# Performance work log

Hardware: AMD Instinct MI355X
Metric: run time of the kernel (lower is better)

The kernel has to match this reference:

```python
import jax, jax.numpy as jnp
import numpy as np

# Model constants (from opt / init_kwargs)
DELTT = 5.0          # temporal resolution [s]
N_TIME = 60          # number of time frames
TR = 5.0             # repetition time
FA = 10.0            # flip angle [deg]
R1 = 4.5             # contrast-agent relaxivity
EPS = 1e-8
SCALE_KTRANS = 1.0
SCALE_VP = 1.0
SCALE_VE = 1.0


def setup_inputs() -> dict:
    key = jax.random.key(0)
    k1, k2, k3, k4 = jax.random.split(key, 4)
    B, T, H, W = 8, N_TIME, 256, 256
    return {
        "params": jax.random.uniform(k1, (B, 3, H, W), dtype=jnp.float32),
        "Cp": jax.random.uniform(k2, (B, T), dtype=jnp.float32),
        "S0": jax.random.uniform(k3, (B, 1, H, W), dtype=jnp.float32),
        "T1": jax.random.uniform(k4, (B, 1, H, W), dtype=jnp.float32),
    }


def reference(params, Cp, S0, T1):
    # PK parameter maps, each [B,1,H,W]
    Ktrans = params[:, 0:1] / SCALE_KTRANS / 60.0
    vp = params[:, 1:2] / SCALE_VP
    ve = params[:, 2:3] / SCALE_VE
    Kep = Ktrans / (ve + EPS)

    # The original O(T^2) windowed sum
    #   Ce[n] = sum_{m<=n} Cp[m] * exp(-Kep*(n-m)*dt) * dt
    # collapses to the linear recurrence
    #   Ce[n] = Ce[n-1]*exp(-Kep*dt) + Cp[n]*dt
    decay = jnp.exp(-Kep[:, 0] * DELTT)  # [B,H,W]

    def step(c, cp_t):
        c = c * decay + cp_t[:, None, None] * DELTT
        return c, c

    c0 = jnp.zeros_like(decay)
    _, Ce = jax.lax.scan(step, c0, Cp.T)   # [T,B,H,W]
    Ce = jnp.moveaxis(Ce, 0, 1)            # [B,T,H,W]

    # Tissue concentration and SPGR signal equation
    Ct = vp * Cp[:, :, None, None] + Ktrans * Ce
    P = TR / (T1 + EPS)
    Q = R1 * TR * Ct / 1000.0
    cos_fa = float(np.cos(FA * np.pi / 180.0))
    eP = jnp.exp(-P)
    ePQ = jnp.exp(-P - Q)
    St = (1.0 - ePQ) * (1.0 - cos_fa * eP) / ((1.0 - cos_fa * ePQ) * (1.0 - eP) + EPS) * S0
    return St
```

## Files before the change

kernel.cpp:

```cpp
#include <hip/hip_runtime.h>


#define N_TIME 60
#define HW (256 * 256)
#define CHUNKS 4
#define CHUNK_LEN (N_TIME / CHUNKS)
#define PXB 4096

typedef float f32x4 __attribute__((ext_vector_type(4)));

__global__ __launch_bounds__(256, 2) void etofts_kernel(
    const float* __restrict__ params,
    const float* __restrict__ Cp,
    const float* __restrict__ S0,
    const float* __restrict__ T1,
    float* __restrict__ out)
{
    const float DT     = 5.0f;
    const float TR     = 5.0f;
    const float EPS    = 1e-8f;
    const float COS_FA = 0.9848077530122081f;
    const float QC2    = 0.0225f * 1.4426950408889634f;

    const int bx    = blockIdx.x;
    const int b     = bx >> 6;
    const int chunk = (bx >> 4) & 3;
    const int blk   = bx & 15;

    const int w    = threadIdx.x >> 6;
    const int lane = threadIdx.x & 63;
    const int pixw = blk * PXB + w * 1024 + lane * 4;

    const float* p0 = params + ((size_t)b * 3 + 0) * HW + pixw;
    const float* p1 = params + ((size_t)b * 3 + 1) * HW + pixw;
    const float* p2 = params + ((size_t)b * 3 + 2) * HW + pixw;
    const float* ps = S0 + (size_t)b * HW + pixw;
    const float* pt = T1 + (size_t)b * HW + pixw;

    float Kt[16], vp[16], decay[16], Ce[16], eP[16], Kc[16], d0[16], d1[16];

#pragma unroll
    for (int q = 0; q < 4; ++q) {
        const float4 kt4 = *reinterpret_cast<const float4*>(p0 + q * 256);
        const float4 vp4 = *reinterpret_cast<const float4*>(p1 + q * 256);
        const float4 ve4 = *reinterpret_cast<const float4*>(p2 + q * 256);
        const float4 s04 = *reinterpret_cast<const float4*>(ps + q * 256);
        const float4 t14 = *reinterpret_cast<const float4*>(pt + q * 256);
        const float ktv[4] = {kt4.x, kt4.y, kt4.z, kt4.w};
        const float vpv[4] = {vp4.x, vp4.y, vp4.z, vp4.w};
        const float vev[4] = {ve4.x, ve4.y, ve4.z, ve4.w};
        const float s0v[4] = {s04.x, s04.y, s04.z, s04.w};
        const float t1v[4] = {t14.x, t14.y, t14.z, t14.w};
#pragma unroll
        for (int i = 0; i < 4; ++i) {
            const int j = q * 4 + i;
            const float Ktrans = ktv[i] * (1.0f / 60.0f);
            const float Kep    = __fdividef(Ktrans, vev[i] + EPS);
            Kt[j]    = Ktrans;
            vp[j]    = vpv[i];
            decay[j] = __expf(-Kep * DT);
            const float P = __fdividef(TR, t1v[i] + EPS);
            const float e = __expf(-P);
            eP[j] = e;
            Kc[j] = (1.0f - COS_FA * e) * s0v[i];
            const float den1 = 1.0f - e;
            d0[j] = den1 + EPS;
            d1[j] = COS_FA * den1;
            Ce[j] = 0.0f;
        }
    }

    const float* cp_row = Cp + b * N_TIME;
    const int t0 = chunk * CHUNK_LEN;

    for (int t = 0; t < t0; ++t) {
        const float cpdt = cp_row[t] * DT;
#pragma unroll
        for (int j = 0; j < 16; ++j) Ce[j] = Ce[j] * decay[j] + cpdt;
    }

    float* outp = out + ((size_t)(b * N_TIME + t0)) * HW + pixw;

#pragma unroll
    for (int k = 0; k < CHUNK_LEN; ++k) {
        const float cp   = cp_row[t0 + k];
        const float cpdt = cp * DT;
        float* op = outp + (size_t)k * HW;
#pragma unroll
        for (int q = 0; q < 4; ++q) {
            float st[4];
#pragma unroll
            for (int i = 0; i < 4; ++i) {
                const int j = q * 4 + i;
                Ce[j] = Ce[j] * decay[j] + cpdt;
                const float Ct  = vp[j] * cp + Kt[j] * Ce[j];
                const float ePQ = eP[j] * exp2f(-QC2 * Ct);
                const float num = Kc[j] - Kc[j] * ePQ;
                const float den = d0[j] - d1[j] * ePQ;
                st[i] = __fdividef(num, den);
            }
            f32x4 v = {st[0], st[1], st[2], st[3]};
            __builtin_nontemporal_store(v, reinterpret_cast<f32x4*>(op + q * 256));
        }
    }
}

extern "C" void kernel_launch(void* const* d_in, const int* in_sizes, int n_in,
                              void* d_out, int out_size, void* d_ws, size_t ws_size,
                              hipStream_t stream) {
    const float* params = (const float*)d_in[0];
    const float* Cp     = (const float*)d_in[1];
    const float* S0     = (const float*)d_in[2];
    const float* T1     = (const float*)d_in[3];
    float* out          = (float*)d_out;

    const int grid = 8 * CHUNKS * (HW / PXB);
    etofts_kernel<<<grid, 256, 0, stream>>>(params, Cp, S0, T1, out);
}
```

Before: 33.11 us.

## Drop time chunking and process full time series per thread with fewer pixels

Removes the split of the time axis into four chunks, each of which recomputed the recurrence prefix, and has every thread run the whole 60-step recurrence for 8 pixels instead of 16. The grid shrinks from 512 to 256 blocks, register pressure per thread falls, and the min-blocks launch bound is dropped. The redundant prefix work goes away, but there is less parallelism across the GPU's compute units and each thread now runs a longer serial chain.

```diff
diff --git a/kernel.cpp b/kernel.cpp
--- a/kernel.cpp
+++ b/kernel.cpp
@@ -3,13 +3,13 @@
 
 #define N_TIME 60
 #define HW (256 * 256)
-#define CHUNKS 4
-#define CHUNK_LEN (N_TIME / CHUNKS)
-#define PXB 4096
+#define PX 8
+#define TPB 256
+#define GRID 256
 
 typedef float f32x4 __attribute__((ext_vector_type(4)));
 
-__global__ __launch_bounds__(256, 2) void etofts_kernel(
+__global__ __launch_bounds__(TPB) void etofts_kernel(
     const float* __restrict__ params,
     const float* __restrict__ Cp,
     const float* __restrict__ S0,
@@ -22,14 +22,13 @@
     const float COS_FA = 0.9848077530122081f;
     const float QC2    = 0.0225f * 1.4426950408889634f;
 
-    const int bx    = blockIdx.x;
-    const int b     = bx >> 6;
-    const int chunk = (bx >> 4) & 3;
-    const int blk   = bx & 15;
+    const int bx  = blockIdx.x;
+    const int b   = bx >> 5;
+    const int blk = bx & 31;
 
     const int w    = threadIdx.x >> 6;
     const int lane = threadIdx.x & 63;
-    const int pixw = blk * PXB + w * 1024 + lane * 4;
+    const int pixw = blk * 2048 + w * 512 + lane * 4;
 
     const float* p0 = params + ((size_t)b * 3 + 0) * HW + pixw;
     const float* p1 = params + ((size_t)b * 3 + 1) * HW + pixw;
@@ -37,10 +36,10 @@
     const float* ps = S0 + (size_t)b * HW + pixw;
     const float* pt = T1 + (size_t)b * HW + pixw;
 
-    float Kt[16], vp[16], decay[16], Ce[16], eP[16], Kc[16], d0[16], d1[16];
+    float Kt[PX], vp[PX], decay[PX], Ce[PX], eP[PX], Kc[PX], d0[PX], d1[PX];
 
 #pragma unroll
-    for (int q = 0; q < 4; ++q) {
+    for (int q = 0; q < 2; ++q) {
         const float4 kt4 = *reinterpret_cast<const float4*>(p0 + q * 256);
         const float4 vp4 = *reinterpret_cast<const float4*>(p1 + q * 256);
         const float4 ve4 = *reinterpret_cast<const float4*>(p2 + q * 256);
@@ -71,23 +70,15 @@
     }
 
     const float* cp_row = Cp + b * N_TIME;
-    const int t0 = chunk * CHUNK_LEN;
+    float* outp = out + ((size_t)b * N_TIME) * HW + pixw;
 
-    for (int t = 0; t < t0; ++t) {
-        const float cpdt = cp_row[t] * DT;
+#pragma unroll 4
+    for (int t = 0; t < N_TIME; ++t) {
+        const float cp   = cp_row[t];
+        const float cpdt = cp * DT;
+        float* op = outp + (size_t)t * HW;
 #pragma unroll
-        for (int j = 0; j < 16; ++j) Ce[j] = Ce[j] * decay[j] + cpdt;
-    }
-
-    float* outp = out + ((size_t)(b * N_TIME + t0)) * HW + pixw;
-
-#pragma unroll
-    for (int k = 0; k < CHUNK_LEN; ++k) {
-        const float cp   = cp_row[t0 + k];
-        const float cpdt = cp * DT;
-        float* op = outp + (size_t)k * HW;
-#pragma unroll
-        for (int q = 0; q < 4; ++q) {
+        for (int q = 0; q < 2; ++q) {
             float st[4];
 #pragma unroll
             for (int i = 0; i < 4; ++i) {
@@ -114,6 +105,5 @@
     const float* T1     = (const float*)d_in[3];
     float* out          = (float*)d_out;
 
-    const int grid = 8 * CHUNKS * (HW / PXB);
-    etofts_kernel<<<grid, 256, 0, stream>>>(params, Cp, S0, T1, out);
+    etofts_kernel<<<GRID, TPB, 0, stream>>>(params, Cp, S0, T1, out);
 }
```

Result: no change. 33.50 us (+1.2%).
